# Kernel optimization log

Measured on AMD Instinct MI355X. Metric: run time of the kernel, lower is better.

The kernel has to match this reference:

```python
import jax, jax.numpy as jnp
import numpy as np

NQ, NL, QD, LD, H = 100000, 32, 384, 1024, 128
E, E_SEE, E_PRED = 1000000, 750000, 250000
N = NQ + NL
EPS = 1e-5


def _bn(x, g, b):
    # BatchNorm1d in training mode: biased batch statistics over node dim
    mu = x.mean(0)
    var = x.var(0)
    return g * (x - mu) * jax.lax.rsqrt(var + EPS) + b


def _general_conv(x, src, dst, ea, Wm, bm, We, be_):
    # PyG GeneralConv (heads=1, no attention, aggr='add', in==out -> identity skip)
    msg = x[src] @ Wm + bm + ea @ We + be_            # [E_see, H]
    agg = jax.ops.segment_sum(msg, dst, num_segments=N)
    return agg + x


def setup_inputs() -> dict:
    key = jax.random.key(0)
    ks = jax.random.split(key, 20)
    s = lambda fan_in: 1.0 / np.sqrt(fan_in)
    return {
        'query_features': jax.random.normal(ks[0], (NQ, QD), jnp.float32),
        'llm_features': jax.random.normal(ks[1], (NL, LD), jnp.float32),
        'edge_index': jax.random.randint(ks[2], (2, E), 0, N, jnp.int64 if jax.config.jax_enable_x64 else jnp.int32),
        'edge_mask': jax.random.randint(ks[3], (E_PRED,), 0, E),
        'edge_can_see': jax.random.randint(ks[4], (E_SEE,), 0, E),
        'edge_weight': jax.random.uniform(ks[5], (E, 1), jnp.float32),
        'Wq': jax.random.normal(ks[6], (QD, H), jnp.float32) * s(QD),
        'bq': jnp.zeros((H,), jnp.float32),
        'Wl': jax.random.normal(ks[7], (LD, H), jnp.float32) * s(LD),
        'bl': jnp.zeros((H,), jnp.float32),
        'W_em': jax.random.normal(ks[8], (1, 1), jnp.float32),
        'b_em': jnp.zeros((1,), jnp.float32),
        'W1m': jax.random.normal(ks[9], (H, H), jnp.float32) * s(H),
        'b1m': jnp.zeros((H,), jnp.float32),
        'W1e': jax.random.normal(ks[10], (1, H), jnp.float32),
        'b1e': jnp.zeros((H,), jnp.float32),
        'W2m': jax.random.normal(ks[11], (H, H), jnp.float32) * s(H),
        'b2m': jnp.zeros((H,), jnp.float32),
        'W2e': jax.random.normal(ks[12], (1, H), jnp.float32),
        'b2e': jnp.zeros((H,), jnp.float32),
        'g1': jnp.ones((H,), jnp.float32), 'beta1': jnp.zeros((H,), jnp.float32),
        'g2': jnp.ones((H,), jnp.float32), 'beta2': jnp.zeros((H,), jnp.float32),
    }


def reference(query_features, llm_features, edge_index, edge_mask, edge_can_see,
              edge_weight, Wq, bq, Wl, bl, W_em, b_em, W1m, b1m, W1e, b1e,
              W2m, b2m, W2e, b2e, g1, beta1, g2, beta2):
    lrelu = jax.nn.leaky_relu  # slope 0.01 (torch default)
    ei_mask = edge_index[:, edge_can_see]       # [2, E_see]
    ei_pred = edge_index[:, edge_mask]          # [2, E_pred]
    ew = lrelu(edge_weight[edge_can_see] @ W_em + b_em)  # [E_see, 1]
    # feature alignment
    x_ini = jnp.concatenate([query_features @ Wq + bq, llm_features @ Wl + bl], 0)  # [N, H]
    src, dst = ei_mask[0], ei_mask[1]
    x = lrelu(_bn(_general_conv(x_ini, src, dst, ew, W1m, b1m, W1e, b1e), g1, beta1))
    x = _bn(_general_conv(x, src, dst, ew, W2m, b2m, W2e, b2e), g2, beta2)
    edge_predict = jax.nn.sigmoid((x_ini[ei_pred[0]] * x[ei_pred[1]]).mean(-1))  # [E_pred]
    return edge_predict
```

## Files before the change

### kernel.cpp

```cpp
#include <hip/hip_runtime.h>
#include <math.h>

#define NQ 100000
#define NL 32
#define QD 384
#define LD 1024
#define H 128
#define E_TOT 1000000
#define E_SEE 750000
#define E_PRED 250000
#define NN (NQ + NL)
#define EPS 1e-5f

#define NB_SCAN ((NN + 255) / 256)
#define NB_G64 (NN / 64)
#define NB_X64 ((NQ + 63) / 64)

typedef __attribute__((ext_vector_type(8))) short short8;
typedef __attribute__((ext_vector_type(4))) short short4v;
typedef __attribute__((ext_vector_type(4))) float f32x4;

__device__ __forceinline__ unsigned short f2bf(float f) {
  unsigned int u = __builtin_bit_cast(unsigned int, f);
  u = (u + 0x7FFFu + ((u >> 16) & 1u)) >> 16;
  return (unsigned short)u;
}


__global__ void k_ew_hist(const int* __restrict__ ecs, const int* __restrict__ EI,
                          const float* __restrict__ ewt, const float* __restrict__ Wem,
                          const float* __restrict__ bem, float* __restrict__ ew,
                          int* __restrict__ cnt, int2* __restrict__ se) {
  int e = blockIdx.x * 256 + threadIdx.x;
  if (e >= E_SEE) return;
  int idx = ecs[e];
  int s = EI[idx];
  int d = EI[E_TOT + idx];
  se[e] = make_int2(s, d);
  atomicAdd(&cnt[d], 1);
  float w = ewt[idx] * Wem[0] + bem[0];
  ew[e] = w > 0.f ? w : 0.01f * w;
}

__global__ void k_scan_block(const int* __restrict__ cnt, int* __restrict__ bsum) {
  __shared__ int red[256];
  int i = blockIdx.x * 256 + threadIdx.x;
  red[threadIdx.x] = (i < NN) ? cnt[i] : 0;
  __syncthreads();
  for (int s = 128; s > 0; s >>= 1) {
    if (threadIdx.x < s) red[threadIdx.x] += red[threadIdx.x + s];
    __syncthreads();
  }
  if (threadIdx.x == 0) bsum[blockIdx.x] = red[0];
}

__global__ void k_scan_top(const int* __restrict__ bsum, int* __restrict__ boff) {
  __shared__ int buf[2][512];
  int t = threadIdx.x;
  int v = (t < NB_SCAN) ? bsum[t] : 0;
  buf[0][t] = v;
  __syncthreads();
  int src = 0;
  for (int d = 1; d < 512; d <<= 1) {
    int x = buf[src][t];
    if (t >= d) x += buf[src][t - d];
    buf[src ^ 1][t] = x;
    __syncthreads();
    src ^= 1;
  }
  if (t < NB_SCAN) boff[t] = buf[src][t] - v;
}

__global__ void k_scan_write(const int* __restrict__ cnt, const int* __restrict__ boff,
                             int* __restrict__ off) {
  __shared__ int buf[2][256];
  int t = threadIdx.x;
  int i = blockIdx.x * 256 + t;
  int v = (i < NN) ? cnt[i] : 0;
  buf[0][t] = v;
  __syncthreads();
  int src = 0;
  for (int d = 1; d < 256; d <<= 1) {
    int x = buf[src][t];
    if (t >= d) x += buf[src][t - d];
    buf[src ^ 1][t] = x;
    __syncthreads();
    src ^= 1;
  }
  if (i < NN) off[i] = boff[blockIdx.x] + buf[src][t] - v;
  if (i == 0) off[NN] = E_SEE;
}

__global__ void k_fill(const int2* __restrict__ se, const float* __restrict__ ew,
                       const int* __restrict__ off, int* __restrict__ cur,
                       int* __restrict__ csr_src, float* __restrict__ csr_ew) {
  int e = blockIdx.x * 256 + threadIdx.x;
  if (e >= E_SEE) return;
  int2 sd = se[e];
  int p = off[sd.y] + atomicAdd(&cur[sd.y], 1);
  csr_src[p] = sd.x;
  csr_ew[p] = ew[e];
}


__global__ void k_prep(const float* __restrict__ Wq, const float* __restrict__ W1m,
                       const float* __restrict__ W2m,
                       unsigned short* __restrict__ Wqt, unsigned short* __restrict__ W1t,
                       unsigned short* __restrict__ W2t) {
  int i = blockIdx.x * 256 + threadIdx.x;
  const int tot1 = QD * H;
  const int tot2 = H * H;
  if (i < tot1) {
    int n = i / QD, k = i - n * QD;
    Wqt[i] = f2bf(Wq[(size_t)k * H + n]);
  } else if (i < tot1 + tot2) {
    int j = i - tot1;
    int n = j >> 7, k = j & 127;
    W1t[j] = f2bf(W1m[(size_t)k * H + n]);
  } else if (i < tot1 + 2 * tot2) {
    int j = i - tot1 - tot2;
    int n = j >> 7, k = j & 127;
    W2t[j] = f2bf(W2m[(size_t)k * H + n]);
  }
}


__global__ __launch_bounds__(128) void k_llm_part(const float* __restrict__ lf,
                                                  const float* __restrict__ Wl,
                                                  float* __restrict__ part) {
  int r = blockIdx.x >> 3;
  int s = blockIdx.x & 7;
  int t = threadIdx.x;
  int k0 = s * 128;
  float acc = 0.f;
#pragma unroll 4
  for (int k = 0; k < 128; k += 4) {
    float a0 = lf[(size_t)r * LD + k0 + k + 0];
    float a1 = lf[(size_t)r * LD + k0 + k + 1];
    float a2 = lf[(size_t)r * LD + k0 + k + 2];
    float a3 = lf[(size_t)r * LD + k0 + k + 3];
    acc = fmaf(a0, Wl[(size_t)(k0 + k + 0) * H + t], acc);
    acc = fmaf(a1, Wl[(size_t)(k0 + k + 1) * H + t], acc);
    acc = fmaf(a2, Wl[(size_t)(k0 + k + 2) * H + t], acc);
    acc = fmaf(a3, Wl[(size_t)(k0 + k + 3) * H + t], acc);
  }
  part[(size_t)blockIdx.x * 128 + t] = acc;
}

__global__ void k_llm_comb(const float* __restrict__ part, const float* __restrict__ bl,
                           float* __restrict__ XINI) {
  int i = blockIdx.x * 256 + threadIdx.x;
  if (i >= NL * H) return;
  int r = i >> 7, t = i & 127;
  float a = bl[t];
#pragma unroll
  for (int s = 0; s < 8; s++) a += part[(size_t)(r * 8 + s) * 128 + t];
  XINI[(size_t)(NQ + r) * H + t] = a;
}


__global__ __launch_bounds__(256) void k_xini(
    const float* __restrict__ qf, const unsigned short* __restrict__ Wqt,
    const float* __restrict__ bq, float* __restrict__ XINI) {
  __shared__ unsigned short sA[64][40];
  __shared__ unsigned short sB[128][40];
  int tid = threadIdx.x;
  int w = tid >> 6, lane = tid & 63;
  int l15 = lane & 15, quad = lane >> 4;
  int wn = (w >> 1) * 32;
  int wm = (w & 1) * 64;
  int rowbase = blockIdx.x * 64;
  f32x4 acc[2][4];
#pragma unroll
  for (int i = 0; i < 2; i++)
#pragma unroll
    for (int j = 0; j < 4; j++) acc[i][j] = (f32x4){0.f, 0.f, 0.f, 0.f};

  int arow = tid >> 3, akc = (tid & 7) * 4;
  int bn = tid >> 2, bk8 = (tid & 3) * 8;
  float4 pa[2];
  int4 pb[2];
#pragma unroll
  for (int p = 0; p < 2; ++p) {
    int gr = rowbase + p * 32 + arow;
    pa[p] = (gr < NQ) ? *(const float4*)&qf[(size_t)gr * QD + akc]
                      : make_float4(0.f, 0.f, 0.f, 0.f);
  }
#pragma unroll
  for (int p = 0; p < 2; ++p)
    pb[p] = *(const int4*)&Wqt[(size_t)(p * 64 + bn) * QD + bk8];

  for (int step = 0; step < 12; ++step) {
#pragma unroll
    for (int p = 0; p < 2; ++p) {
      short4v b;
      b.x = (short)f2bf(pa[p].x); b.y = (short)f2bf(pa[p].y);
      b.z = (short)f2bf(pa[p].z); b.w = (short)f2bf(pa[p].w);
      *(short4v*)&sA[p * 32 + arow][akc] = b;
    }
#pragma unroll
    for (int p = 0; p < 2; ++p) *(int4*)&sB[p * 64 + bn][bk8] = pb[p];
    __syncthreads();
    if (step + 1 < 12) {
      int kn = (step + 1) * 32;
#pragma unroll
      for (int p = 0; p < 2; ++p) {
        int gr = rowbase + p * 32 + arow;
        pa[p] = (gr < NQ) ? *(const float4*)&qf[(size_t)gr * QD + kn + akc]
                          : make_float4(0.f, 0.f, 0.f, 0.f);
      }
#pragma unroll
      for (int p = 0; p < 2; ++p)
        pb[p] = *(const int4*)&Wqt[(size_t)(p * 64 + bn) * QD + kn + bk8];
    }
    short8 af[4], bfr[2];
#pragma unroll
    for (int mt = 0; mt < 4; ++mt)
      af[mt] = *(const short8*)&sB[wm + mt * 16 + l15][quad * 8];
#pragma unroll
    for (int nt = 0; nt < 2; ++nt)
      bfr[nt] = *(const short8*)&sA[wn + nt * 16 + l15][quad * 8];
#pragma unroll
    for (int nt = 0; nt < 2; ++nt)
#pragma unroll
      for (int mt = 0; mt < 4; ++mt)
        acc[nt][mt] = __builtin_amdgcn_mfma_f32_16x16x32_bf16(
            af[mt], bfr[nt], acc[nt][mt], 0, 0, 0);
    __syncthreads();
  }
#pragma unroll
  for (int nt = 0; nt < 2; ++nt) {
    int row = rowbase + wn + nt * 16 + l15;
    if (row < NQ) {
#pragma unroll
      for (int mt = 0; mt < 4; ++mt) {
        int cb = wm + mt * 16 + quad * 4;
        float4 bias = *(const float4*)&bq[cb];
        float4 o = make_float4(acc[nt][mt][0] + bias.x, acc[nt][mt][1] + bias.y,
                               acc[nt][mt][2] + bias.z, acc[nt][mt][3] + bias.w);
        *(float4*)&XINI[(size_t)row * H + cb] = o;
      }
    }
  }
}


template <bool TRANS>
__global__ __launch_bounds__(256) void k_seg(
    const float* __restrict__ Xin, const int* __restrict__ off,
    const int* __restrict__ csr_src, const float* __restrict__ csr_ew,
    const float* __restrict__ scale, const float* __restrict__ shift,
    unsigned short* __restrict__ S16, float* __restrict__ swsum,
    float* __restrict__ degf) {
  int w = blockIdx.x * 4 + (threadIdx.x >> 6);
  if (w >= NN) return;
  int lane = threadIdx.x & 63;
  int o0 = off[w], o1 = off[w + 1];
  float ax = 1.f, ay = 1.f, bx = 0.f, by = 0.f;
  if (TRANS) {
    float2 sc = *(const float2*)&scale[lane * 2];
    float2 sh = *(const float2*)&shift[lane * 2];
    ax = sc.x; ay = sc.y; bx = sh.x; by = sh.y;
  }
  float accx = 0.f, accy = 0.f, ews = 0.f;
  for (int k = o0; k < o1; ++k) {
    int s = csr_src[k];
    float2 v = *(const float2*)&Xin[(size_t)s * H + lane * 2];
    if (TRANS) {
      float t0 = fmaf(ax, v.x, bx); v.x = t0 > 0.f ? t0 : 0.01f * t0;
      float t1 = fmaf(ay, v.y, by); v.y = t1 > 0.f ? t1 : 0.01f * t1;
    }
    accx += v.x; accy += v.y;
    ews += csr_ew[k];
  }
  unsigned int pk = ((unsigned int)f2bf(accy) << 16) | f2bf(accx);
  *(unsigned int*)&S16[(size_t)w * H + lane * 2] = pk;
  if (lane == 0) { swsum[w] = ews; degf[w] = (float)(o1 - o0); }
}


template <bool TRANS>
__global__ __launch_bounds__(256) void k_gemm(
    const unsigned short* __restrict__ S16, const float* __restrict__ Xin,
    float* __restrict__ Xout, const unsigned short* __restrict__ Wt,
    const float* __restrict__ bm, const float* __restrict__ be,
    const float* __restrict__ We,
    const float* __restrict__ scale, const float* __restrict__ shift,
    const float* __restrict__ swsum, const float* __restrict__ degf,
    float* __restrict__ partials) {
  __shared__ unsigned short sA[64][40];
  __shared__ unsigned short sB[128][40];
  __shared__ float st[2][2][128];
  int tid = threadIdx.x;
  int w = tid >> 6, lane = tid & 63;
  int l15 = lane & 15, quad = lane >> 4;
  int wn = (w >> 1) * 32, wm = (w & 1) * 64;
  int rowbase = blockIdx.x * 64;
  f32x4 acc[2][4];
#pragma unroll
  for (int i = 0; i < 2; i++)
#pragma unroll
    for (int j = 0; j < 4; j++) acc[i][j] = (f32x4){0.f, 0.f, 0.f, 0.f};

  int arow = tid >> 2, ak8 = (tid & 3) * 8;
  int bn = tid >> 2, bk8 = (tid & 3) * 8;
  int4 pa;
  int4 pb[2];
  pa = *(const int4*)&S16[(size_t)(rowbase + arow) * H + ak8];
#pragma unroll
  for (int p = 0; p < 2; ++p)
    pb[p] = *(const int4*)&Wt[(size_t)(p * 64 + bn) * H + bk8];

  for (int step = 0; step < 4; ++step) {
    *(int4*)&sA[arow][ak8] = pa;
#pragma unroll
    for (int p = 0; p < 2; ++p) *(int4*)&sB[p * 64 + bn][bk8] = pb[p];
    __syncthreads();
    if (step + 1 < 4) {
      int kn = (step + 1) * 32;
      pa = *(const int4*)&S16[(size_t)(rowbase + arow) * H + kn + ak8];
#pragma unroll
      for (int p = 0; p < 2; ++p)
        pb[p] = *(const int4*)&Wt[(size_t)(p * 64 + bn) * H + kn + bk8];
    }
    short8 af[4], bfr[2];
#pragma unroll
    for (int mt = 0; mt < 4; ++mt)
      af[mt] = *(const short8*)&sB[wm + mt * 16 + l15][quad * 8];
#pragma unroll
    for (int nt = 0; nt < 2; ++nt)
      bfr[nt] = *(const short8*)&sA[wn + nt * 16 + l15][quad * 8];
#pragma unroll
    for (int nt = 0; nt < 2; ++nt)
#pragma unroll
      for (int mt = 0; mt < 4; ++mt)
        acc[nt][mt] = __builtin_amdgcn_mfma_f32_16x16x32_bf16(
            af[mt], bfr[nt], acc[nt][mt], 0, 0, 0);
    __syncthreads();
  }
  int n0 = rowbase + wn + l15;
  float dg0 = degf[n0], sw0 = swsum[n0];
  float dg1 = degf[n0 + 16], sw1 = swsum[n0 + 16];
#pragma unroll
  for (int mt = 0; mt < 4; ++mt) {
    int cb = wm + mt * 16 + quad * 4;
    float4 m4 = *(const float4*)&bm[cb];
    float4 e4 = *(const float4*)&be[cb];
    float4 cb4 = make_float4(m4.x + e4.x, m4.y + e4.y, m4.z + e4.z, m4.w + e4.w);
    float4 we4 = *(const float4*)&We[cb];
    float4 sc4, sh4;
    if (TRANS) { sc4 = *(const float4*)&scale[cb]; sh4 = *(const float4*)&shift[cb]; }
    f32x4 psum = {0.f, 0.f, 0.f, 0.f}, psq = {0.f, 0.f, 0.f, 0.f};
#pragma unroll
    for (int nt = 0; nt < 2; ++nt) {
      int n = n0 + nt * 16;
      float dg = nt ? dg1 : dg0, sw = nt ? sw1 : sw0;
      float4 rr = *(const float4*)&Xin[(size_t)n * H + cb];
      if (TRANS) {
        float t;
        t = fmaf(sc4.x, rr.x, sh4.x); rr.x = t > 0.f ? t : 0.01f * t;
        t = fmaf(sc4.y, rr.y, sh4.y); rr.y = t > 0.f ? t : 0.01f * t;
        t = fmaf(sc4.z, rr.z, sh4.z); rr.z = t > 0.f ? t : 0.01f * t;
        t = fmaf(sc4.w, rr.w, sh4.w); rr.w = t > 0.f ? t : 0.01f * t;
      }
      float4 o;
      o.x = acc[nt][mt][0] + dg * cb4.x + sw * we4.x + rr.x;
      o.y = acc[nt][mt][1] + dg * cb4.y + sw * we4.y + rr.y;
      o.z = acc[nt][mt][2] + dg * cb4.z + sw * we4.z + rr.z;
      o.w = acc[nt][mt][3] + dg * cb4.w + sw * we4.w + rr.w;
      *(float4*)&Xout[(size_t)n * H + cb] = o;
      psum[0] += o.x; psum[1] += o.y; psum[2] += o.z; psum[3] += o.w;
      psq[0] += o.x * o.x; psq[1] += o.y * o.y; psq[2] += o.z * o.z; psq[3] += o.w * o.w;
    }
#pragma unroll
    for (int s = 1; s < 16; s <<= 1) {
#pragma unroll
      for (int j = 0; j < 4; ++j) {
        psum[j] += __shfl_xor(psum[j], s, 64);
        psq[j] += __shfl_xor(psq[j], s, 64);
      }
    }
    if (l15 == 0) {
      *(f32x4*)&st[0][w >> 1][cb] = psum;
      *(f32x4*)&st[1][w >> 1][cb] = psq;
    }
  }
  __syncthreads();
  int stat = tid >> 7, col = tid & 127;
  partials[(size_t)blockIdx.x * 256 + tid] = st[stat][0][col] + st[stat][1][col];
}


__global__ __launch_bounds__(256) void k_bnstats(
    const float* __restrict__ partials, const float* __restrict__ g,
    const float* __restrict__ beta, float* __restrict__ scale,
    float* __restrict__ shift) {
  __shared__ float rs[256], rq[256];
  int j = blockIdx.x;
  int t = threadIdx.x;
  float as = 0.f, aq = 0.f;
  for (int b = t; b < NB_G64; b += 256) {
    as += partials[(size_t)b * 256 + j];
    aq += partials[(size_t)b * 256 + 128 + j];
  }
  rs[t] = as; rq[t] = aq;
  __syncthreads();
  for (int s = 128; s > 0; s >>= 1) {
    if (t < s) { rs[t] += rs[t + s]; rq[t] += rq[t + s]; }
    __syncthreads();
  }
  if (t == 0) {
    float mean = rs[0] / (float)NN;
    float var = rq[0] / (float)NN - mean * mean;
    float a = g[j] * rsqrtf(var + EPS);
    scale[j] = a;
    shift[j] = beta[j] - mean * a;
  }
}


__global__ __launch_bounds__(256) void k_pred(
    const int* __restrict__ emask, const int* __restrict__ EI,
    const float* __restrict__ XINI, const float* __restrict__ X,
    const float* __restrict__ scale, const float* __restrict__ shift,
    float* __restrict__ out) {
  int i = blockIdx.x * 4 + (threadIdx.x >> 6);
  if (i >= E_PRED) return;
  int lane = threadIdx.x & 63;
  int m = emask[i];
  int p0 = EI[m];
  int p1 = EI[E_TOT + m];
  float2 a = *(const float2*)&XINI[(size_t)p0 * H + lane * 2];
  float2 b = *(const float2*)&X[(size_t)p1 * H + lane * 2];
  float2 sc = *(const float2*)&scale[lane * 2];
  float2 sh = *(const float2*)&shift[lane * 2];
  float v = a.x * fmaf(sc.x, b.x, sh.x) + a.y * fmaf(sc.y, b.y, sh.y);
#pragma unroll
  for (int mm = 32; mm > 0; mm >>= 1) v += __shfl_xor(v, mm, 64);
  if (lane == 0) out[i] = 1.f / (1.f + expf(-v * (1.f / 128.f)));
}


extern "C" void kernel_launch(void* const* d_in, const int* in_sizes, int n_in,
                              void* d_out, int out_size, void* d_ws, size_t ws_size,
                              hipStream_t stream) {
  const float* qf    = (const float*)d_in[0];
  const float* lf    = (const float*)d_in[1];
  const int*   EI    = (const int*)d_in[2];
  const int*   emask = (const int*)d_in[3];
  const int*   ecs   = (const int*)d_in[4];
  const float* ewt   = (const float*)d_in[5];
  const float* Wq    = (const float*)d_in[6];
  const float* bq    = (const float*)d_in[7];
  const float* Wl    = (const float*)d_in[8];
  const float* bl    = (const float*)d_in[9];
  const float* Wem   = (const float*)d_in[10];
  const float* bem   = (const float*)d_in[11];
  const float* W1m   = (const float*)d_in[12];
  const float* b1m   = (const float*)d_in[13];
  const float* W1e   = (const float*)d_in[14];
  const float* b1e   = (const float*)d_in[15];
  const float* W2m   = (const float*)d_in[16];
  const float* b2m   = (const float*)d_in[17];
  const float* W2e   = (const float*)d_in[18];
  const float* b2e   = (const float*)d_in[19];
  const float* g1    = (const float*)d_in[20];
  const float* beta1 = (const float*)d_in[21];
  const float* g2    = (const float*)d_in[22];
  const float* beta2 = (const float*)d_in[23];
  float* out = (float*)d_out;

  char* p = (char*)d_ws;
  auto alloc = [&](size_t bytes) -> void* {
    void* r = (void*)p;
    p += (bytes + 255) & ~(size_t)255;
    return r;
  };
  float* XINI    = (float*)alloc((size_t)NN * H * 4);
  float* X       = (float*)alloc((size_t)NN * H * 4);
  unsigned short* S16 = (unsigned short*)alloc((size_t)NN * H * 2);
  float* ew      = (float*)alloc((size_t)E_SEE * 4);
  float* csr_ew  = (float*)alloc((size_t)E_SEE * 4);
  int*   csr_src = (int*)alloc((size_t)E_SEE * 4);
  int2*  se      = (int2*)alloc((size_t)E_SEE * 8);
  int*   cnt     = (int*)alloc((size_t)NN * 4);
  int*   off     = (int*)alloc((size_t)(NN + 1) * 4);
  int*   cur     = (int*)alloc((size_t)NN * 4);
  int*   bsum    = (int*)alloc((size_t)NB_SCAN * 4);
  int*   boff    = (int*)alloc((size_t)NB_SCAN * 4);
  float* swsum   = (float*)alloc((size_t)NN * 4);
  float* degf    = (float*)alloc((size_t)NN * 4);
  float* partials= (float*)alloc((size_t)NB_G64 * 256 * 4);
  float* scale1  = (float*)alloc(128 * 4);
  float* shift1  = (float*)alloc(128 * 4);
  float* scale2  = (float*)alloc(128 * 4);
  float* shift2  = (float*)alloc(128 * 4);
  unsigned short* Wqt = (unsigned short*)alloc((size_t)QD * H * 2);
  unsigned short* W1t = (unsigned short*)alloc((size_t)H * H * 2);
  unsigned short* W2t = (unsigned short*)alloc((size_t)H * H * 2);
  float* llmpart = (float*)alloc((size_t)NL * 8 * H * 4);

  hipMemsetAsync(cnt, 0, (size_t)NN * 4, stream);
  hipMemsetAsync(cur, 0, (size_t)NN * 4, stream);

  int ebl = (E_SEE + 255) / 256;
  k_prep<<<320, 256, 0, stream>>>(Wq, W1m, W2m, Wqt, W1t, W2t);
  k_ew_hist<<<ebl, 256, 0, stream>>>(ecs, EI, ewt, Wem, bem, ew, cnt, se);
  k_scan_block<<<NB_SCAN, 256, 0, stream>>>(cnt, bsum);
  k_scan_top<<<1, 512, 0, stream>>>(bsum, boff);
  k_scan_write<<<NB_SCAN, 256, 0, stream>>>(cnt, boff, off);
  k_fill<<<ebl, 256, 0, stream>>>(se, ew, off, cur, csr_src, csr_ew);

  k_llm_part<<<NL * 8, 128, 0, stream>>>(lf, Wl, llmpart);
  k_llm_comb<<<(NL * H + 255) / 256, 256, 0, stream>>>(llmpart, bl, XINI);
  k_xini<<<NB_X64, 256, 0, stream>>>(qf, Wqt, bq, XINI);

  int segbl = (NN + 3) / 4;
  k_seg<false><<<segbl, 256, 0, stream>>>(XINI, off, csr_src, csr_ew,
                                          nullptr, nullptr, S16, swsum, degf);
  k_gemm<false><<<NB_G64, 256, 0, stream>>>(S16, XINI, X, W1t, b1m, b1e, W1e,
                                            nullptr, nullptr, swsum, degf, partials);
  k_bnstats<<<H, 256, 0, stream>>>(partials, g1, beta1, scale1, shift1);
  k_seg<true><<<segbl, 256, 0, stream>>>(X, off, csr_src, csr_ew,
                                         scale1, shift1, S16, swsum, degf);
  k_gemm<true><<<NB_G64, 256, 0, stream>>>(S16, X, X, W2t, b2m, b2e, W2e,
                                           scale1, shift1, swsum, degf, partials);
  k_bnstats<<<H, 256, 0, stream>>>(partials, g2, beta2, scale2, shift2);
  int pbl = (E_PRED + 3) / 4;
  k_pred<<<pbl, 256, 0, stream>>>(emask, EI, XINI, X, scale2, shift2, out);
}
```

Before: 736.1 us.

## Store node features in bf16 and load MFMA operands directly from global

Node feature buffers XINI and X change from fp32 to bf16, which halves the bytes moved by the random-gather segment kernels, the GEMM residual reads and the prediction gathers. The xini and gemm kernels drop their LDS staging and barriers and load MFMA fragments straight from global memory. This lowers memory traffic and synchronisation. The cost is extra rounding of intermediate activations and less coalesced fragment loads.

```diff
diff --git a/kernel.cpp b/kernel.cpp
--- a/kernel.cpp
+++ b/kernel.cpp
@@ -17,13 +17,21 @@
 #define NB_X64 ((NQ + 63) / 64)
 
 typedef __attribute__((ext_vector_type(8))) short short8;
-typedef __attribute__((ext_vector_type(4))) short short4v;
 typedef __attribute__((ext_vector_type(4))) float f32x4;
 
 __device__ __forceinline__ unsigned short f2bf(float f) {
   unsigned int u = __builtin_bit_cast(unsigned int, f);
   u = (u + 0x7FFFu + ((u >> 16) & 1u)) >> 16;
   return (unsigned short)u;
+}
+__device__ __forceinline__ float bflo(unsigned int u) {
+  return __builtin_bit_cast(float, u << 16);
+}
+__device__ __forceinline__ float bfhi(unsigned int u) {
+  return __builtin_bit_cast(float, u & 0xFFFF0000u);
+}
+__device__ __forceinline__ unsigned int pk2(float a, float b) {
+  return ((unsigned int)f2bf(b) << 16) | f2bf(a);
 }
 
 
@@ -148,97 +156,74 @@
 }
 
 __global__ void k_llm_comb(const float* __restrict__ part, const float* __restrict__ bl,
-                           float* __restrict__ XINI) {
+                           unsigned short* __restrict__ XINI16) {
   int i = blockIdx.x * 256 + threadIdx.x;
   if (i >= NL * H) return;
   int r = i >> 7, t = i & 127;
   float a = bl[t];
 #pragma unroll
   for (int s = 0; s < 8; s++) a += part[(size_t)(r * 8 + s) * 128 + t];
-  XINI[(size_t)(NQ + r) * H + t] = a;
+  XINI16[(size_t)(NQ + r) * H + t] = f2bf(a);
 }
 
 
 __global__ __launch_bounds__(256) void k_xini(
     const float* __restrict__ qf, const unsigned short* __restrict__ Wqt,
-    const float* __restrict__ bq, float* __restrict__ XINI) {
-  __shared__ unsigned short sA[64][40];
-  __shared__ unsigned short sB[128][40];
+    const float* __restrict__ bq, unsigned short* __restrict__ XINI16) {
   int tid = threadIdx.x;
   int w = tid >> 6, lane = tid & 63;
   int l15 = lane & 15, quad = lane >> 4;
   int wn = (w >> 1) * 32;
   int wm = (w & 1) * 64;
   int rowbase = blockIdx.x * 64;
+  int rowq = rowbase + wn + l15;
   f32x4 acc[2][4];
 #pragma unroll
   for (int i = 0; i < 2; i++)
 #pragma unroll
     for (int j = 0; j < 4; j++) acc[i][j] = (f32x4){0.f, 0.f, 0.f, 0.f};
 
-  int arow = tid >> 3, akc = (tid & 7) * 4;
-  int bn = tid >> 2, bk8 = (tid & 3) * 8;
-  float4 pa[2];
-  int4 pb[2];
-#pragma unroll
-  for (int p = 0; p < 2; ++p) {
-    int gr = rowbase + p * 32 + arow;
-    pa[p] = (gr < NQ) ? *(const float4*)&qf[(size_t)gr * QD + akc]
-                      : make_float4(0.f, 0.f, 0.f, 0.f);
-  }
-#pragma unroll
-  for (int p = 0; p < 2; ++p)
-    pb[p] = *(const int4*)&Wqt[(size_t)(p * 64 + bn) * QD + bk8];
-
-  for (int step = 0; step < 12; ++step) {
-#pragma unroll
-    for (int p = 0; p < 2; ++p) {
-      short4v b;
-      b.x = (short)f2bf(pa[p].x); b.y = (short)f2bf(pa[p].y);
-      b.z = (short)f2bf(pa[p].z); b.w = (short)f2bf(pa[p].w);
-      *(short4v*)&sA[p * 32 + arow][akc] = b;
-    }
-#pragma unroll
-    for (int p = 0; p < 2; ++p) *(int4*)&sB[p * 64 + bn][bk8] = pb[p];
-    __syncthreads();
-    if (step + 1 < 12) {
-      int kn = (step + 1) * 32;
-#pragma unroll
-      for (int p = 0; p < 2; ++p) {
-        int gr = rowbase + p * 32 + arow;
-        pa[p] = (gr < NQ) ? *(const float4*)&qf[(size_t)gr * QD + kn + akc]
-                          : make_float4(0.f, 0.f, 0.f, 0.f);
+#pragma unroll 3
+  for (int s = 0; s < 12; ++s) {
+    int k0 = s * 32 + quad * 8;
+    short8 af[4];
+#pragma unroll
+    for (int mt = 0; mt < 4; ++mt)
+      af[mt] = *(const short8*)&Wqt[(size_t)(wm + mt * 16 + l15) * QD + k0];
+    short8 bfr[2];
+#pragma unroll
+    for (int nt = 0; nt < 2; ++nt) {
+      int r = rowq + nt * 16;
+      float4 f0 = make_float4(0.f, 0.f, 0.f, 0.f), f1 = f0;
+      if (r < NQ) {
+        f0 = *(const float4*)&qf[(size_t)r * QD + k0];
+        f1 = *(const float4*)&qf[(size_t)r * QD + k0 + 4];
       }
-#pragma unroll
-      for (int p = 0; p < 2; ++p)
-        pb[p] = *(const int4*)&Wqt[(size_t)(p * 64 + bn) * QD + kn + bk8];
-    }
-    short8 af[4], bfr[2];
-#pragma unroll
-    for (int mt = 0; mt < 4; ++mt)
-      af[mt] = *(const short8*)&sB[wm + mt * 16 + l15][quad * 8];
-#pragma unroll
-    for (int nt = 0; nt < 2; ++nt)
-      bfr[nt] = *(const short8*)&sA[wn + nt * 16 + l15][quad * 8];
+      short8 b;
+      b[0] = (short)f2bf(f0.x); b[1] = (short)f2bf(f0.y);
+      b[2] = (short)f2bf(f0.z); b[3] = (short)f2bf(f0.w);
+      b[4] = (short)f2bf(f1.x); b[5] = (short)f2bf(f1.y);
+      b[6] = (short)f2bf(f1.z); b[7] = (short)f2bf(f1.w);
+      bfr[nt] = b;
+    }
 #pragma unroll
     for (int nt = 0; nt < 2; ++nt)
 #pragma unroll
       for (int mt = 0; mt < 4; ++mt)
         acc[nt][mt] = __builtin_amdgcn_mfma_f32_16x16x32_bf16(
             af[mt], bfr[nt], acc[nt][mt], 0, 0, 0);
-    __syncthreads();
   }
 #pragma unroll
   for (int nt = 0; nt < 2; ++nt) {
-    int row = rowbase + wn + nt * 16 + l15;
+    int row = rowq + nt * 16;
     if (row < NQ) {
 #pragma unroll
       for (int mt = 0; mt < 4; ++mt) {
         int cb = wm + mt * 16 + quad * 4;
         float4 bias = *(const float4*)&bq[cb];
-        float4 o = make_float4(acc[nt][mt][0] + bias.x, acc[nt][mt][1] + bias.y,
-                               acc[nt][mt][2] + bias.z, acc[nt][mt][3] + bias.w);
-        *(float4*)&XINI[(size_t)row * H + cb] = o;
+        uint2 pk = make_uint2(pk2(acc[nt][mt][0] + bias.x, acc[nt][mt][1] + bias.y),
+                              pk2(acc[nt][mt][2] + bias.z, acc[nt][mt][3] + bias.w));
+        *(uint2*)&XINI16[(size_t)row * H + cb] = pk;
       }
     }
   }
@@ -247,7 +232,7 @@
 
 template <bool TRANS>
 __global__ __launch_bounds__(256) void k_seg(
-    const float* __restrict__ Xin, const int* __restrict__ off,
+    const unsigned short* __restrict__ X16, const int* __restrict__ off,
     const int* __restrict__ csr_src, const float* __restrict__ csr_ew,
     const float* __restrict__ scale, const float* __restrict__ shift,
     unsigned short* __restrict__ S16, float* __restrict__ swsum,
@@ -265,82 +250,62 @@
   float accx = 0.f, accy = 0.f, ews = 0.f;
   for (int k = o0; k < o1; ++k) {
     int s = csr_src[k];
-    float2 v = *(const float2*)&Xin[(size_t)s * H + lane * 2];
+    unsigned int pk = *(const unsigned int*)&X16[(size_t)s * H + lane * 2];
+    float vx = bflo(pk), vy = bfhi(pk);
     if (TRANS) {
-      float t0 = fmaf(ax, v.x, bx); v.x = t0 > 0.f ? t0 : 0.01f * t0;
-      float t1 = fmaf(ay, v.y, by); v.y = t1 > 0.f ? t1 : 0.01f * t1;
-    }
-    accx += v.x; accy += v.y;
+      float t0 = fmaf(ax, vx, bx); vx = t0 > 0.f ? t0 : 0.01f * t0;
+      float t1 = fmaf(ay, vy, by); vy = t1 > 0.f ? t1 : 0.01f * t1;
+    }
+    accx += vx; accy += vy;
     ews += csr_ew[k];
   }
-  unsigned int pk = ((unsigned int)f2bf(accy) << 16) | f2bf(accx);
-  *(unsigned int*)&S16[(size_t)w * H + lane * 2] = pk;
+  *(unsigned int*)&S16[(size_t)w * H + lane * 2] = pk2(accx, accy);
   if (lane == 0) { swsum[w] = ews; degf[w] = (float)(o1 - o0); }
 }
 
 
 template <bool TRANS>
 __global__ __launch_bounds__(256) void k_gemm(
-    const unsigned short* __restrict__ S16, const float* __restrict__ Xin,
-    float* __restrict__ Xout, const unsigned short* __restrict__ Wt,
+    const unsigned short* __restrict__ S16, const unsigned short* __restrict__ Xin16,
+    unsigned short* __restrict__ Xout16,
+    const unsigned short* __restrict__ Wt,
     const float* __restrict__ bm, const float* __restrict__ be,
     const float* __restrict__ We,
     const float* __restrict__ scale, const float* __restrict__ shift,
     const float* __restrict__ swsum, const float* __restrict__ degf,
     float* __restrict__ partials) {
-  __shared__ unsigned short sA[64][40];
-  __shared__ unsigned short sB[128][40];
   __shared__ float st[2][2][128];
   int tid = threadIdx.x;
   int w = tid >> 6, lane = tid & 63;
   int l15 = lane & 15, quad = lane >> 4;
   int wn = (w >> 1) * 32, wm = (w & 1) * 64;
   int rowbase = blockIdx.x * 64;
+  int rowq = rowbase + wn + l15;
   f32x4 acc[2][4];
 #pragma unroll
   for (int i = 0; i < 2; i++)
 #pragma unroll
     for (int j = 0; j < 4; j++) acc[i][j] = (f32x4){0.f, 0.f, 0.f, 0.f};
 
-  int arow = tid >> 2, ak8 = (tid & 3) * 8;
-  int bn = tid >> 2, bk8 = (tid & 3) * 8;
-  int4 pa;
-  int4 pb[2];
-  pa = *(const int4*)&S16[(size_t)(rowbase + arow) * H + ak8];
-#pragma unroll
-  for (int p = 0; p < 2; ++p)
-    pb[p] = *(const int4*)&Wt[(size_t)(p * 64 + bn) * H + bk8];
-
-  for (int step = 0; step < 4; ++step) {
-    *(int4*)&sA[arow][ak8] = pa;
-#pragma unroll
-    for (int p = 0; p < 2; ++p) *(int4*)&sB[p * 64 + bn][bk8] = pb[p];
-    __syncthreads();
-    if (step + 1 < 4) {
-      int kn = (step + 1) * 32;
-      pa = *(const int4*)&S16[(size_t)(rowbase + arow) * H + kn + ak8];
-#pragma unroll
-      for (int p = 0; p < 2; ++p)
-        pb[p] = *(const int4*)&Wt[(size_t)(p * 64 + bn) * H + kn + bk8];
-    }
+#pragma unroll
+  for (int s = 0; s < 4; ++s) {
+    int k0 = s * 32 + quad * 8;
     short8 af[4], bfr[2];
 #pragma unroll
     for (int mt = 0; mt < 4; ++mt)
-      af[mt] = *(const short8*)&sB[wm + mt * 16 + l15][quad * 8];
+      af[mt] = *(const short8*)&Wt[(size_t)(wm + mt * 16 + l15) * H + k0];
 #pragma unroll
     for (int nt = 0; nt < 2; ++nt)
-      bfr[nt] = *(const short8*)&sA[wn + nt * 16 + l15][quad * 8];
+      bfr[nt] = *(const short8*)&S16[(size_t)(rowq + nt * 16) * H + k0];
 #pragma unroll
     for (int nt = 0; nt < 2; ++nt)
 #pragma unroll
       for (int mt = 0; mt < 4; ++mt)
         acc[nt][mt] = __builtin_amdgcn_mfma_f32_16x16x32_bf16(
             af[mt], bfr[nt], acc[nt][mt], 0, 0, 0);
-    __syncthreads();
-  }
-  int n0 = rowbase + wn + l15;
-  float dg0 = degf[n0], sw0 = swsum[n0];
-  float dg1 = degf[n0 + 16], sw1 = swsum[n0 + 16];
+  }
+  float dg0 = degf[rowq], sw0 = swsum[rowq];
+  float dg1 = degf[rowq + 16], sw1 = swsum[rowq + 16];
 #pragma unroll
   for (int mt = 0; mt < 4; ++mt) {
     int cb = wm + mt * 16 + quad * 4;
@@ -353,9 +318,10 @@
     f32x4 psum = {0.f, 0.f, 0.f, 0.f}, psq = {0.f, 0.f, 0.f, 0.f};
 #pragma unroll
     for (int nt = 0; nt < 2; ++nt) {
-      int n = n0 + nt * 16;
+      int n = rowq + nt * 16;
       float dg = nt ? dg1 : dg0, sw = nt ? sw1 : sw0;
-      float4 rr = *(const float4*)&Xin[(size_t)n * H + cb];
+      uint2 pr = *(const uint2*)&Xin16[(size_t)n * H + cb];
+      float4 rr = make_float4(bflo(pr.x), bfhi(pr.x), bflo(pr.y), bfhi(pr.y));
       if (TRANS) {
         float t;
         t = fmaf(sc4.x, rr.x, sh4.x); rr.x = t > 0.f ? t : 0.01f * t;
@@ -368,7 +334,8 @@
       o.y = acc[nt][mt][1] + dg * cb4.y + sw * we4.y + rr.y;
       o.z = acc[nt][mt][2] + dg * cb4.z + sw * we4.z + rr.z;
       o.w = acc[nt][mt][3] + dg * cb4.w + sw * we4.w + rr.w;
-      *(float4*)&Xout[(size_t)n * H + cb] = o;
+      uint2 pk = make_uint2(pk2(o.x, o.y), pk2(o.z, o.w));
+      *(uint2*)&Xout16[(size_t)n * H + cb] = pk;
       psum[0] += o.x; psum[1] += o.y; psum[2] += o.z; psum[3] += o.w;
       psq[0] += o.x * o.x; psq[1] += o.y * o.y; psq[2] += o.z * o.z; psq[3] += o.w * o.w;
     }
@@ -421,7 +388,7 @@
 
 __global__ __launch_bounds__(256) void k_pred(
     const int* __restrict__ emask, const int* __restrict__ EI,
-    const float* __restrict__ XINI, const float* __restrict__ X,
+    const unsigned short* __restrict__ XINI16, const unsigned short* __restrict__ X16,
     const float* __restrict__ scale, const float* __restrict__ shift,
     float* __restrict__ out) {
   int i = blockIdx.x * 4 + (threadIdx.x >> 6);
@@ -430,11 +397,12 @@
   int m = emask[i];
   int p0 = EI[m];
   int p1 = EI[E_TOT + m];
-  float2 a = *(const float2*)&XINI[(size_t)p0 * H + lane * 2];
-  float2 b = *(const float2*)&X[(size_t)p1 * H + lane * 2];
+  unsigned int pa = *(const unsigned int*)&XINI16[(size_t)p0 * H + lane * 2];
+  unsigned int pb = *(const unsigned int*)&X16[(size_t)p1 * H + lane * 2];
   float2 sc = *(const float2*)&scale[lane * 2];
   float2 sh = *(const float2*)&shift[lane * 2];
-  float v = a.x * fmaf(sc.x, b.x, sh.x) + a.y * fmaf(sc.y, b.y, sh.y);
+  float v = bflo(pa) * fmaf(sc.x, bflo(pb), sh.x) +
+            bfhi(pa) * fmaf(sc.y, bfhi(pb), sh.y);
 #pragma unroll
   for (int mm = 32; mm > 0; mm >>= 1) v += __shfl_xor(v, mm, 64);
   if (lane == 0) out[i] = 1.f / (1.f + expf(-v * (1.f / 128.f)));
@@ -476,9 +444,9 @@
     p += (bytes + 255) & ~(size_t)255;
     return r;
   };
-  float* XINI    = (float*)alloc((size_t)NN * H * 4);
-  float* X       = (float*)alloc((size_t)NN * H * 4);
-  unsigned short* S16 = (unsigned short*)alloc((size_t)NN * H * 2);
+  unsigned short* XINI16 = (unsigned short*)alloc((size_t)NN * H * 2);
+  unsigned short* X16    = (unsigned short*)alloc((size_t)NN * H * 2);
+  unsigned short* S16    = (unsigned short*)alloc((size_t)NN * H * 2);
   float* ew      = (float*)alloc((size_t)E_SEE * 4);
   float* csr_ew  = (float*)alloc((size_t)E_SEE * 4);
   int*   csr_src = (int*)alloc((size_t)E_SEE * 4);
@@ -512,20 +480,20 @@
   k_fill<<<ebl, 256, 0, stream>>>(se, ew, off, cur, csr_src, csr_ew);
 
   k_llm_part<<<NL * 8, 128, 0, stream>>>(lf, Wl, llmpart);
-  k_llm_comb<<<(NL * H + 255) / 256, 256, 0, stream>>>(llmpart, bl, XINI);
-  k_xini<<<NB_X64, 256, 0, stream>>>(qf, Wqt, bq, XINI);
+  k_llm_comb<<<(NL * H + 255) / 256, 256, 0, stream>>>(llmpart, bl, XINI16);
+  k_xini<<<NB_X64, 256, 0, stream>>>(qf, Wqt, bq, XINI16);
 
   int segbl = (NN + 3) / 4;
-  k_seg<false><<<segbl, 256, 0, stream>>>(XINI, off, csr_src, csr_ew,
+  k_seg<false><<<segbl, 256, 0, stream>>>(XINI16, off, csr_src, csr_ew,
                                           nullptr, nullptr, S16, swsum, degf);
-  k_gemm<false><<<NB_G64, 256, 0, stream>>>(S16, XINI, X, W1t, b1m, b1e, W1e,
+  k_gemm<false><<<NB_G64, 256, 0, stream>>>(S16, XINI16, X16, W1t, b1m, b1e, W1e,
                                             nullptr, nullptr, swsum, degf, partials);
   k_bnstats<<<H, 256, 0, stream>>>(partials, g1, beta1, scale1, shift1);
-  k_seg<true><<<segbl, 256, 0, stream>>>(X, off, csr_src, csr_ew,
+  k_seg<true><<<segbl, 256, 0, stream>>>(X16, off, csr_src, csr_ew,
                                          scale1, shift1, S16, swsum, degf);
-  k_gemm<true><<<NB_G64, 256, 0, stream>>>(S16, X, X, W2t, b2m, b2e, W2e,
+  k_gemm<true><<<NB_G64, 256, 0, stream>>>(S16, X16, X16, W2t, b2m, b2e, W2e,
                                            scale1, shift1, swsum, degf, partials);
   k_bnstats<<<H, 256, 0, stream>>>(partials, g2, beta2, scale2, shift2);
   int pbl = (E_PRED + 3) / 4;
-  k_pred<<<pbl, 256, 0, stream>>>(emask, EI, XINI, X, scale2, shift2, out);
-}
+  k_pred<<<pbl, 256, 0, stream>>>(emask, EI, XINI16, X16, scale2, shift2, out);
+}
```

Measured after the change: 728.7 us. No clear change (-1.0%).
